# Performance work log

Hardware: AMD Instinct MI355X
Metric: run time of the kernel (lower is better)

Reference implementation:

```python
import jax, jax.numpy as jnp
import numpy as np
from jax import lax

C_IN, C_OUT, K, N_BASE, HIDDEN = 256, 256, 3, 8, 128
ATT_TAU = 1.0


def setup_inputs() -> dict:
    key = jax.random.key(0)
    ks = jax.random.split(key, 6)
    B, H, W = 64, 64, 64
    x = jax.random.normal(ks[0], (B, C_IN, H, W), dtype=jnp.float32)
    # attention MLP params (torch Linear convention: W is [out, in])
    w1 = jax.random.normal(ks[1], (HIDDEN, C_IN), dtype=jnp.float32) * (1.0 / np.sqrt(C_IN))
    b1 = jnp.zeros((HIDDEN,), dtype=jnp.float32)
    w2 = jax.random.normal(ks[2], (C_OUT * N_BASE, HIDDEN), dtype=jnp.float32) * (1.0 / np.sqrt(HIDDEN))
    b2 = jnp.zeros((C_OUT * N_BASE,), dtype=jnp.float32)
    # base filters: kaiming-normal over flat [n_base, c_in*k*k]
    fan_in = C_IN * K * K
    base_filters = jax.random.normal(ks[3], (N_BASE, fan_in), dtype=jnp.float32) * np.sqrt(2.0 / fan_in)
    return {"x": x, "w1": w1, "b1": b1, "w2": w2, "b2": b2, "base_filters": base_filters}


def reference(x, w1, b1, w2, b2, base_filters):
    B = x.shape[0]
    # global average pool -> [B, c_in]
    pooled = x.mean(axis=(2, 3))
    # attention MLP -> per-sample mixing weights [B, c_out, n_base]
    h = jax.nn.relu(pooled @ w1.T + b1)
    mix = (h @ w2.T + b2).reshape(B, C_OUT, N_BASE)
    mix = jax.nn.softmax(mix / ATT_TAU, axis=2)
    # base conv: [B, c_in, H, W] -> [B, n_base, H, W], SAME padding (k//2)
    filt = base_filters.reshape(N_BASE, C_IN, K, K)
    pad = K // 2
    y = lax.conv_general_dilated(
        x, filt, window_strides=(1, 1), padding=[(pad, pad), (pad, pad)],
        dimension_numbers=("NCHW", "OIHW", "NCHW"))
    # per-sample 1x1 mixing conv == batched matmul over channels
    out = jnp.einsum("bon,bnhw->bohw", mix, y)
    return out
```

## Files before the change

### kernel.cpp

```cpp
#include <hip/hip_runtime.h>
#include <math.h>

#define CIN 256
#define COUT 256
#define NB 8
#define HID 128
#define HW 4096
#define BATCH 64

#define TROWS 18
#define XSTR 68

typedef float f32x4 __attribute__((ext_vector_type(4)));

__global__ __launch_bounds__(256) void repack_filters(
    const float* __restrict__ bf, float* __restrict__ fT) {
  int i = blockIdx.x * 256 + threadIdx.x;
  if (i < 8 * 2304) {
    int n = i / 2304;
    int cd = i % 2304;
    fT[cd * 8 + n] = bf[i];
  }
}

__global__ __launch_bounds__(256, 4) void conv_pool_kernel(
    const float* __restrict__ x, const float* __restrict__ fT,
    float* __restrict__ ypart, float* __restrict__ poolpart) {
  __shared__ float xs[8 * TROWS * XSTR];
  const int t = threadIdx.x;
  const int bid = blockIdx.x;
  const int b = bid >> 4;
  const int g = (bid >> 2) & 3;
  const int rc = bid & 3;
  const int row0 = rc * 16;
  const int c0 = g * 64;

  const int ch = t >> 5;
  const int part = t & 31;
  const int p16 = part >> 4;
  const int seg = part & 15;
  const int r = t >> 4;
  const int cg = t & 15;

  float4 v[9];
  {
    const float* xsrc0 = x + ((size_t)(b * CIN + c0 + ch) * HW);
#pragma unroll
    for (int i = 0; i < 9; ++i) {
      const int grow = row0 - 1 + 2 * i + p16;
      if ((unsigned)grow < 64u)
        v[i] = *(const float4*)(xsrc0 + grow * 64 + seg * 4);
    }
  }

  for (int i = t; i < 8 * TROWS * XSTR; i += 256) xs[i] = 0.0f;

  float acc[8][4];
#pragma unroll
  for (int n = 0; n < 8; ++n)
#pragma unroll
    for (int j = 0; j < 4; ++j) acc[n][j] = 0.0f;

#pragma unroll 1
  for (int chunk = 0; chunk < 8; ++chunk) {
    const int cbase = c0 + chunk * 8;

    __syncthreads();

    float psum = 0.0f;
#pragma unroll
    for (int i = 0; i < 9; ++i) {
      const int row = 2 * i + p16;
      const int grow = row0 - 1 + row;
      if ((unsigned)grow < 64u) {
        float* dst = &xs[(ch * TROWS + row) * XSTR + 1 + seg * 4];
        dst[0] = v[i].x; dst[1] = v[i].y; dst[2] = v[i].z; dst[3] = v[i].w;
        if (row >= 1 && row <= 16)
          psum += (v[i].x + v[i].y) + (v[i].z + v[i].w);
      }
    }
#pragma unroll
    for (int off = 16; off > 0; off >>= 1)
      psum += __shfl_down(psum, off, 32);
    if (part == 0)
      poolpart[(b * 4 + rc) * 256 + cbase + ch] = psum;
    __syncthreads();

    if (chunk < 7) {
      const float* xsrc = x + ((size_t)(b * CIN + cbase + 8 + ch) * HW);
#pragma unroll
      for (int i = 0; i < 9; ++i) {
        const int grow = row0 - 1 + 2 * i + p16;
        if ((unsigned)grow < 64u)
          v[i] = *(const float4*)(xsrc + grow * 64 + seg * 4);
      }
    }

#pragma unroll
    for (int cc = 0; cc < 8; ++cc) {
      const float* fb = fT + (size_t)(cbase + cc) * 72;
      const float* xrow = &xs[(cc * TROWS + r) * XSTR + cg * 4];
#pragma unroll
      for (int dy = 0; dy < 3; ++dy) {
        const float* xr = xrow + dy * XSTR;
        float4 a0 = *(const float4*)(xr);
        float2 a1 = *(const float2*)(xr + 4);
        float w[6];
        w[0] = a0.x; w[1] = a0.y; w[2] = a0.z; w[3] = a0.w;
        w[4] = a1.x; w[5] = a1.y;
#pragma unroll
        for (int dx = 0; dx < 3; ++dx) {
#pragma unroll
          for (int n = 0; n < 8; ++n) {
            const float fv = fb[(dy * 3 + dx) * 8 + n];
#pragma unroll
            for (int j = 0; j < 4; ++j)
              acc[n][j] = fmaf(w[j + dx], fv, acc[n][j]);
          }
        }
      }
    }
  }

#pragma unroll
  for (int n = 0; n < 8; ++n) {
    float* yp = ypart +
        ((size_t)(((b * 4 + g) * 8 + n) * 64 + row0 + r) * 64 + cg * 4);
    float4 v0 = {acc[n][0], acc[n][1], acc[n][2], acc[n][3]};
    *(float4*)(yp) = v0;
  }
}

__global__ __launch_bounds__(256) void mlp_kernel(
    const float* __restrict__ poolpart, const float* __restrict__ w1,
    const float* __restrict__ b1, const float* __restrict__ w2,
    const float* __restrict__ b2, float* __restrict__ mix) {
  __shared__ float pool_s[256];
  __shared__ float h_s[128];
  const int t = threadIdx.x;
  const int b = blockIdx.x;
  pool_s[t] = (poolpart[(b * 4 + 0) * 256 + t] +
               poolpart[(b * 4 + 1) * 256 + t] +
               poolpart[(b * 4 + 2) * 256 + t] +
               poolpart[(b * 4 + 3) * 256 + t]) * (1.0f / 4096.0f);
  __syncthreads();
  if (t < 128) {
    float a = b1[t];
    const float* wr = w1 + t * 256;
    for (int c = 0; c < 256; c += 4) {
      float4 wv = *(const float4*)(wr + c);
      a = fmaf(pool_s[c], wv.x, a);
      a = fmaf(pool_s[c + 1], wv.y, a);
      a = fmaf(pool_s[c + 2], wv.z, a);
      a = fmaf(pool_s[c + 3], wv.w, a);
    }
    h_s[t] = fmaxf(a, 0.0f);
  }
  __syncthreads();
  float m[8];
#pragma unroll
  for (int n = 0; n < 8; ++n) {
    float a = b2[t * 8 + n];
    const float* wr = w2 + (size_t)(t * 8 + n) * 128;
    for (int j = 0; j < 128; j += 4) {
      float4 wv = *(const float4*)(wr + j);
      a = fmaf(h_s[j], wv.x, a);
      a = fmaf(h_s[j + 1], wv.y, a);
      a = fmaf(h_s[j + 2], wv.z, a);
      a = fmaf(h_s[j + 3], wv.w, a);
    }
    m[n] = a;
  }
  float mx = m[0];
#pragma unroll
  for (int n = 1; n < 8; ++n) mx = fmaxf(mx, m[n]);
  float s = 0.0f;
#pragma unroll
  for (int n = 0; n < 8; ++n) {
    m[n] = __expf(m[n] - mx);
    s += m[n];
  }
  float inv = 1.0f / s;
#pragma unroll
  for (int n = 0; n < 8; ++n) mix[(size_t)(b * 256 + t) * 8 + n] = m[n] * inv;
}

__global__ __launch_bounds__(256, 4) void mix_conv_kernel(
    const float* __restrict__ ypart, const float* __restrict__ mix,
    float* __restrict__ out) {
  __shared__ float ys[8 * 1024];
  const int t = threadIdx.x;
  const int bid = blockIdx.x;
  const int b = bid >> 3;
  const int tile = (bid >> 1) & 3;
  const int oh = bid & 1;
  const int p0 = tile * 1024;

  const float* yb = ypart + (size_t)b * 4 * 8 * HW + p0;
  for (int i = t; i < 2048; i += 256) {
    int n = i >> 8;
    int pv = i & 255;
    const float* y0 = yb + n * HW + pv * 4;
    float4 a = *(const float4*)(y0);
    float4 c = *(const float4*)(y0 + 8 * HW);
    float4 d = *(const float4*)(y0 + 16 * HW);
    float4 e = *(const float4*)(y0 + 24 * HW);
    float4 rr = {a.x + c.x + d.x + e.x, a.y + c.y + d.y + e.y,
                 a.z + c.z + d.z + e.z, a.w + c.w + d.w + e.w};
    *(float4*)&ys[n * 1024 + pv * 4] = rr;
  }
  __syncthreads();

  float4 y4[8];
#pragma unroll
  for (int n = 0; n < 8; ++n) y4[n] = *(const float4*)&ys[n * 1024 + t * 4];

  const float* mixb = mix + ((size_t)b * 256 + oh * 128) * 8;
  float* op = out + ((size_t)b * COUT + oh * 128) * HW + p0 + t * 4;
#pragma unroll 2
  for (int o = 0; o < 128; ++o) {
    const float* mp = mixb + o * 8;
    float4 ma = *(const float4*)(mp);
    float4 mb = *(const float4*)(mp + 4);
    float4 r;
    r.x = ma.x * y4[0].x; r.y = ma.x * y4[0].y;
    r.z = ma.x * y4[0].z; r.w = ma.x * y4[0].w;
    r.x = fmaf(ma.y, y4[1].x, r.x); r.y = fmaf(ma.y, y4[1].y, r.y);
    r.z = fmaf(ma.y, y4[1].z, r.z); r.w = fmaf(ma.y, y4[1].w, r.w);
    r.x = fmaf(ma.z, y4[2].x, r.x); r.y = fmaf(ma.z, y4[2].y, r.y);
    r.z = fmaf(ma.z, y4[2].z, r.z); r.w = fmaf(ma.z, y4[2].w, r.w);
    r.x = fmaf(ma.w, y4[3].x, r.x); r.y = fmaf(ma.w, y4[3].y, r.y);
    r.z = fmaf(ma.w, y4[3].z, r.z); r.w = fmaf(ma.w, y4[3].w, r.w);
    r.x = fmaf(mb.x, y4[4].x, r.x); r.y = fmaf(mb.x, y4[4].y, r.y);
    r.z = fmaf(mb.x, y4[4].z, r.z); r.w = fmaf(mb.x, y4[4].w, r.w);
    r.x = fmaf(mb.y, y4[5].x, r.x); r.y = fmaf(mb.y, y4[5].y, r.y);
    r.z = fmaf(mb.y, y4[5].z, r.z); r.w = fmaf(mb.y, y4[5].w, r.w);
    r.x = fmaf(mb.z, y4[6].x, r.x); r.y = fmaf(mb.z, y4[6].y, r.y);
    r.z = fmaf(mb.z, y4[6].z, r.z); r.w = fmaf(mb.z, y4[6].w, r.w);
    r.x = fmaf(mb.w, y4[7].x, r.x); r.y = fmaf(mb.w, y4[7].y, r.y);
    r.z = fmaf(mb.w, y4[7].z, r.z); r.w = fmaf(mb.w, y4[7].w, r.w);
    f32x4 rn = {r.x, r.y, r.z, r.w};
    __builtin_nontemporal_store(rn, (f32x4*)(op + (size_t)o * HW));
  }
}

extern "C" void kernel_launch(void* const* d_in, const int* in_sizes, int n_in,
                              void* d_out, int out_size, void* d_ws,
                              size_t ws_size, hipStream_t stream) {
  const float* x  = (const float*)d_in[0];
  const float* w1 = (const float*)d_in[1];
  const float* b1 = (const float*)d_in[2];
  const float* w2 = (const float*)d_in[3];
  const float* b2 = (const float*)d_in[4];
  const float* bf = (const float*)d_in[5];
  float* out = (float*)d_out;

  char* ws = (char*)d_ws;
  float* ypart    = (float*)(ws);
  float* poolpart = (float*)(ws + 33554432);
  float* mixw     = (float*)(ws + 33554432 + 262144);
  float* fT       = (float*)(ws + 33554432 + 262144 + 2097152);

  repack_filters<<<72, 256, 0, stream>>>(bf, fT);
  conv_pool_kernel<<<1024, 256, 0, stream>>>(x, fT, ypart, poolpart);
  mlp_kernel<<<64, 256, 0, stream>>>(poolpart, w1, b1, w2, b2, mixw);
  mix_conv_kernel<<<512, 256, 0, stream>>>(ypart, mixw, out);
}
```

Baseline: 607.0 us.

## Replace LDS-staged conv input tile with direct global loads and lane shuffles

The conv kernel no longer stages an 8-channel halo tile in shared memory with double-buffered register prefetch and block barriers. Each thread now loads its own row plus the rows above and below straight from global memory per channel, and gets the left and right halo pixels through intra-16-lane shuffles. Pooling is done per wave with xor shuffles and combined at the end through a small shared array. This removes LDS traffic and the per-chunk __syncthreads, but reads each input row three times from global/L2 with no explicit prefetch, and it drops the occupancy hint from launch bounds.

```diff
diff --git a/kernel.cpp b/kernel.cpp
--- a/kernel.cpp
+++ b/kernel.cpp
@@ -7,9 +7,6 @@
 #define HID 128
 #define HW 4096
 #define BATCH 64
-
-#define TROWS 18
-#define XSTR 68
 
 typedef float f32x4 __attribute__((ext_vector_type(4)));
 
@@ -23,10 +20,10 @@
   }
 }
 
-__global__ __launch_bounds__(256, 4) void conv_pool_kernel(
+__global__ __launch_bounds__(256) void conv_pool_kernel(
     const float* __restrict__ x, const float* __restrict__ fT,
     float* __restrict__ ypart, float* __restrict__ poolpart) {
-  __shared__ float xs[8 * TROWS * XSTR];
+  __shared__ float pools[4][64];
   const int t = threadIdx.x;
   const int bid = blockIdx.x;
   const int b = bid >> 4;
@@ -34,26 +31,10 @@
   const int rc = bid & 3;
   const int row0 = rc * 16;
   const int c0 = g * 64;
-
-  const int ch = t >> 5;
-  const int part = t & 31;
-  const int p16 = part >> 4;
-  const int seg = part & 15;
+  const int w = t >> 6;
   const int r = t >> 4;
   const int cg = t & 15;
-
-  float4 v[9];
-  {
-    const float* xsrc0 = x + ((size_t)(b * CIN + c0 + ch) * HW);
-#pragma unroll
-    for (int i = 0; i < 9; ++i) {
-      const int grow = row0 - 1 + 2 * i + p16;
-      if ((unsigned)grow < 64u)
-        v[i] = *(const float4*)(xsrc0 + grow * 64 + seg * 4);
-    }
-  }
-
-  for (int i = t; i < 8 * TROWS * XSTR; i += 256) xs[i] = 0.0f;
+  const int grow = row0 + r;
 
   float acc[8][4];
 #pragma unroll
@@ -61,66 +42,54 @@
 #pragma unroll
     for (int j = 0; j < 4; ++j) acc[n][j] = 0.0f;
 
-#pragma unroll 1
-  for (int chunk = 0; chunk < 8; ++chunk) {
-    const int cbase = c0 + chunk * 8;
-
-    __syncthreads();
-
-    float psum = 0.0f;
-#pragma unroll
-    for (int i = 0; i < 9; ++i) {
-      const int row = 2 * i + p16;
-      const int grow = row0 - 1 + row;
-      if ((unsigned)grow < 64u) {
-        float* dst = &xs[(ch * TROWS + row) * XSTR + 1 + seg * 4];
-        dst[0] = v[i].x; dst[1] = v[i].y; dst[2] = v[i].z; dst[3] = v[i].w;
-        if (row >= 1 && row <= 16)
-          psum += (v[i].x + v[i].y) + (v[i].z + v[i].w);
-      }
-    }
-#pragma unroll
-    for (int off = 16; off > 0; off >>= 1)
-      psum += __shfl_down(psum, off, 32);
-    if (part == 0)
-      poolpart[(b * 4 + rc) * 256 + cbase + ch] = psum;
-    __syncthreads();
-
-    if (chunk < 7) {
-      const float* xsrc = x + ((size_t)(b * CIN + cbase + 8 + ch) * HW);
-#pragma unroll
-      for (int i = 0; i < 9; ++i) {
-        const int grow = row0 - 1 + 2 * i + p16;
-        if ((unsigned)grow < 64u)
-          v[i] = *(const float4*)(xsrc + grow * 64 + seg * 4);
-      }
-    }
-
-#pragma unroll
-    for (int cc = 0; cc < 8; ++cc) {
-      const float* fb = fT + (size_t)(cbase + cc) * 72;
-      const float* xrow = &xs[(cc * TROWS + r) * XSTR + cg * 4];
-#pragma unroll
-      for (int dy = 0; dy < 3; ++dy) {
-        const float* xr = xrow + dy * XSTR;
-        float4 a0 = *(const float4*)(xr);
-        float2 a1 = *(const float2*)(xr + 4);
-        float w[6];
-        w[0] = a0.x; w[1] = a0.y; w[2] = a0.z; w[3] = a0.w;
-        w[4] = a1.x; w[5] = a1.y;
-#pragma unroll
-        for (int dx = 0; dx < 3; ++dx) {
-#pragma unroll
-          for (int n = 0; n < 8; ++n) {
-            const float fv = fb[(dy * 3 + dx) * 8 + n];
-#pragma unroll
-            for (int j = 0; j < 4; ++j)
-              acc[n][j] = fmaf(w[j + dx], fv, acc[n][j]);
-          }
+  const float* xp = x + ((size_t)(b * CIN + c0) * HW) + grow * 64 + cg * 4;
+  const bool has_up = (grow > 0);
+  const bool has_dn = (grow < 63);
+
+#pragma unroll 2
+  for (int c = 0; c < 64; ++c) {
+    const float* xc = xp + (size_t)c * HW;
+    float4 z4 = {0.0f, 0.0f, 0.0f, 0.0f};
+    float4 a1 = *(const float4*)(xc);
+    float4 a0 = has_up ? *(const float4*)(xc - 64) : z4;
+    float4 a2 = has_dn ? *(const float4*)(xc + 64) : z4;
+
+    float ps = (a1.x + a1.y) + (a1.z + a1.w);
+    ps += __shfl_xor(ps, 8, 16);
+    ps += __shfl_xor(ps, 4, 16);
+    ps += __shfl_xor(ps, 2, 16);
+    ps += __shfl_xor(ps, 1, 16);
+    ps += __shfl_xor(ps, 16, 64);
+    ps += __shfl_xor(ps, 32, 64);
+    if ((t & 63) == 0) pools[w][c] = ps;
+
+    const float* fb = fT + (size_t)(c0 + c) * 72;
+#pragma unroll
+    for (int dy = 0; dy < 3; ++dy) {
+      float4 v4 = (dy == 0) ? a0 : ((dy == 1) ? a1 : a2);
+      float wl = __shfl_up(v4.w, 1, 16);
+      float wr = __shfl_down(v4.x, 1, 16);
+      float w6[6];
+      w6[0] = (cg == 0) ? 0.0f : wl;
+      w6[1] = v4.x; w6[2] = v4.y; w6[3] = v4.z; w6[4] = v4.w;
+      w6[5] = (cg == 15) ? 0.0f : wr;
+#pragma unroll
+      for (int dx = 0; dx < 3; ++dx) {
+#pragma unroll
+        for (int n = 0; n < 8; ++n) {
+          const float fv = fb[(dy * 3 + dx) * 8 + n];
+#pragma unroll
+          for (int j = 0; j < 4; ++j)
+            acc[n][j] = fmaf(w6[j + dx], fv, acc[n][j]);
         }
       }
     }
   }
+
+  __syncthreads();
+  if (t < 64)
+    poolpart[(b * 4 + rc) * 256 + c0 + t] =
+        pools[0][t] + pools[1][t] + pools[2][t] + pools[3][t];
 
 #pragma unroll
   for (int n = 0; n < 8; ++n) {
```

New measurement: 608.4 us. No clear change (+0.2%).
